# Optimization experiments

Hardware: AMD Instinct MI355X
Metric: run time of the kernel (lower is better)

Reference implementation:

```python
import jax, jax.numpy as jnp
import numpy as np

B, SQ, SK, D, H = 2, 2048, 2048, 1024, 16
DK = D // H


def setup_inputs() -> dict:
    key = jax.random.key(0)
    ks = jax.random.split(key, 9)
    query = jax.random.normal(ks[0], (B, SQ, D), dtype=jnp.float32)
    k_in = jax.random.normal(ks[1], (B, SK, D), dtype=jnp.float32)
    v_in = jax.random.normal(ks[2], (B, SK, D), dtype=jnp.float32)
    # padding mask: 1 for valid tokens, 0 for padding; lengths in [SK//2, SK]
    lengths = jax.random.randint(ks[3], (B,), SK // 2, SK + 1)
    mask = (jnp.arange(SK)[None, :] < lengths[:, None]).astype(jnp.int32)
    scale = 1.0 / np.sqrt(D)
    Wq = jax.random.normal(ks[4], (D, D), dtype=jnp.float32) * scale
    Wk = jax.random.normal(ks[5], (D, D), dtype=jnp.float32) * scale
    Wv = jax.random.normal(ks[6], (D, D), dtype=jnp.float32) * scale
    Wo = jax.random.normal(ks[7], (D, D), dtype=jnp.float32) * scale
    return {"query": query, "key": k_in, "value": v_in, "mask": mask,
            "Wq": Wq, "Wk": Wk, "Wv": Wv, "Wo": Wo}


def reference(query, key, value, mask, Wq, Wk, Wv, Wo):
    # linear projections (torch Linear: x @ W.T)
    q = (query @ Wq.T).reshape(B, SQ, H, DK).transpose(0, 2, 1, 3)  # [B,H,SQ,DK]
    k = (key @ Wk.T).reshape(B, SK, H, DK).transpose(0, 2, 1, 3)    # [B,H,SK,DK]
    v = (value @ Wv.T).reshape(B, SK, H, DK).transpose(0, 2, 1, 3)  # [B,H,SK,DK]
    scores = jnp.einsum('bhqd,bhkd->bhqk', q, k) / jnp.sqrt(jnp.float32(DK))
    # padding mask: (B, SK) -> (B, 1, 1, SK)
    scores = jnp.where(mask[:, None, None, :] == 0, -jnp.inf, scores)
    # future (causal) mask
    future = jnp.triu(jnp.ones((SQ, SK), dtype=bool), k=1)
    scores = jnp.where(future[None, None], -jnp.inf, scores)
    attn = jax.nn.softmax(scores, axis=-1)
    attn = jnp.nan_to_num(attn, nan=0.0)
    ctx = jnp.einsum('bhqk,bhkd->bhqd', attn, v)
    ctx = ctx.transpose(0, 2, 1, 3).reshape(B, SQ, D)
    return ctx @ Wo.T
```

## Files before the change

### kernel.cpp

```cpp
#include <hip/hip_runtime.h>
#include <hip/hip_bf16.h>
#include <stdint.h>

#define BB 2
#define SS 2048
#define DD 1024
#define HH 16
#define DKK 64
#define MM (BB*SS)
#define LOG2E 1.4426950408889634f
#define QSCALE (0.125f * LOG2E)

typedef __attribute__((ext_vector_type(8))) short short8;
typedef __attribute__((ext_vector_type(4))) float f32x4;

__device__ __forceinline__ short bfr(float f) {
    return (short)((__float_as_uint(f) + 0x8000u) >> 16);
}
__device__ __forceinline__ short8 cvt8(float4 a, float4 b) {
    short8 s;
    s[0] = bfr(a.x); s[1] = bfr(a.y); s[2] = bfr(a.z); s[3] = bfr(a.w);
    s[4] = bfr(b.x); s[5] = bfr(b.y); s[6] = bfr(b.z); s[7] = bfr(b.w);
    return s;
}

__device__ __forceinline__ void dma16(const void* g, void* l) {
    __builtin_amdgcn_global_load_lds(
        (const __attribute__((address_space(1))) uint32_t*)g,
        (__attribute__((address_space(3))) uint32_t*)(uintptr_t)l, 16, 0, 0);
}


__global__ __launch_bounds__(256) void cvt_all(const float* __restrict__ q,
                                               const float* __restrict__ k,
                                               const float* __restrict__ v,
                                               const float* __restrict__ wq,
                                               const float* __restrict__ wk,
                                               const float* __restrict__ wv,
                                               const float* __restrict__ wo,
                                               const int* __restrict__ mask,
                                               short* __restrict__ dst,
                                               float* __restrict__ Fb) {
    const size_t nth = (size_t)gridDim.x * blockDim.x;
    const size_t tid = (size_t)blockIdx.x * blockDim.x + threadIdx.x;
    if (tid < BB * SS) Fb[tid] = mask[tid] ? 0.f : -30000.f;
    for (size_t i8 = tid; i8 < (1u << 21); i8 += nth) {
        const size_t e = i8 * 8;
        const float* s;
        size_t rel;
        if (e < 4194304)        { s = q; rel = e; }
        else if (e < 8388608)   { s = k; rel = e - 4194304; }
        else if (e < 12582912)  { s = v; rel = e - 8388608; }
        else {
            const size_t we = e - 12582912;
            s = (we < 1048576) ? wq : (we < 2097152) ? wk : (we < 3145728) ? wv : wo;
            rel = we & 1048575;
        }
        const float4* p = (const float4*)(s + rel);
        *(short8*)(dst + e) = cvt8(p[0], p[1]);
    }
}

__global__ __launch_bounds__(256) void qkv_lds(const short* __restrict__ Abf,
                                               const short* __restrict__ Wbf,
                                               short* __restrict__ Qb,
                                               short* __restrict__ Kb,
                                               short* __restrict__ Vtb) {
    __shared__ __align__(16) short As[128 * 64];
    __shared__ __align__(16) short Ws[128 * 64];
    const int z = blockIdx.z;
    const short* A = Abf + (size_t)z * 4194304;
    const short* W = Wbf + (size_t)z * 1048576;
    const int t = threadIdx.x, wave = t >> 6, lane = t & 63;
    const int la = lane & 15, quad = lane >> 4;
    const int wm = wave & 1, wn = wave >> 1;
    const int m0 = blockIdx.x * 128, n0 = blockIdx.y * 128;

    f32x4 acc[4][4];
    #pragma unroll
    for (int i = 0; i < 4; ++i)
        #pragma unroll
        for (int j = 0; j < 4; ++j) acc[i][j] = {0.f, 0.f, 0.f, 0.f};

    for (int k0 = 0; k0 < DD; k0 += 64) {
        #pragma unroll
        for (int j = 0; j < 4; ++j) {
            const int idx = j * 256 + t;
            const int row = idx >> 3, cpos = idx & 7;
            const int gc = cpos ^ (row & 7);
            dma16(A + (size_t)(m0 + row) * DD + k0 + gc * 8, (short*)As + idx * 8);
            dma16(W + (size_t)(n0 + row) * DD + k0 + gc * 8, (short*)Ws + idx * 8);
        }
        __syncthreads();
        #pragma unroll
        for (int kh = 0; kh < 2; ++kh) {
            short8 af[4], bf[4];
            #pragma unroll
            for (int mt = 0; mt < 4; ++mt) {
                const int row = wm * 64 + mt * 16 + la;
                af[mt] = *(const short8*)&As[row * 64 + (((kh << 2) | quad) ^ (row & 7)) * 8];
            }
            #pragma unroll
            for (int nt = 0; nt < 4; ++nt) {
                const int row = wn * 64 + nt * 16 + la;
                bf[nt] = *(const short8*)&Ws[row * 64 + (((kh << 2) | quad) ^ (row & 7)) * 8];
            }
            #pragma unroll
            for (int mt = 0; mt < 4; ++mt)
                #pragma unroll
                for (int nt = 0; nt < 4; ++nt)
                    acc[mt][nt] = __builtin_amdgcn_mfma_f32_16x16x32_bf16(af[mt], bf[nt], acc[mt][nt], 0, 0, 0);
        }
        __syncthreads();
    }

    #pragma unroll
    for (int mt = 0; mt < 4; ++mt)
        #pragma unroll
        for (int nt = 0; nt < 4; ++nt)
            #pragma unroll
            for (int r = 0; r < 4; ++r) {
                const int m = m0 + wm * 64 + mt * 16 + quad * 4 + r;
                const int n = n0 + wn * 64 + nt * 16 + la;
                const int b = m >> 11, s = m & (SS - 1);
                const int h = n >> 6, dk = n & 63;
                const int bh = b * HH + h;
                const float v = acc[mt][nt][r];
                if (z == 0)      Qb[((size_t)bh * SS + s) * DKK + dk] = bfr(v * QSCALE);
                else if (z == 1) Kb[((size_t)bh * SS + s) * DKK + dk] = bfr(v);
                else             Vtb[((size_t)bh * DKK + dk) * SS + s] = bfr(v);
            }
}

__global__ __launch_bounds__(256) void attn3(const short* __restrict__ Q,
                                             const short* __restrict__ K,
                                             const short* __restrict__ Vt,
                                             const float* __restrict__ Fb,
                                             short* __restrict__ ctx) {
    const int b = blockIdx.z, h = blockIdx.y;
    const int qt = 31 - blockIdx.x;
    const int t = threadIdx.x, wave = t >> 6, lane = t & 63;
    const int la = lane & 15, quad = lane >> 4;

    __shared__ __align__(16) short Ks[64][72];
    __shared__ __align__(16) short Vs[64][72];
    __shared__ __align__(16) short Ps[64][72];

    const size_t kbase = ((size_t)(b * HH + h) * SS) * DKK;
    const size_t vbase = ((size_t)(b * HH + h) * DKK) * SS;

    const short8 aq0 = *(const short8*)(Q + kbase + (size_t)(qt * 64 + wave * 16 + la) * DKK + quad * 8);
    const short8 aq1 = *(const short8*)(Q + kbase + (size_t)(qt * 64 + wave * 16 + la) * DKK + 32 + quad * 8);

    const int srow = t >> 2, scol = (t & 3) * 16;
    short8 kr[2], vr[2];
    auto loadG = [&](int kt) {
        const short* kp = K + kbase + (size_t)(kt * 64 + srow) * DKK + scol;
        kr[0] = ((const short8*)kp)[0]; kr[1] = ((const short8*)kp)[1];
        const short* vp = Vt + vbase + (size_t)srow * SS + kt * 64 + scol;
        vr[0] = ((const short8*)vp)[0]; vr[1] = ((const short8*)vp)[1];
    };
    auto storeL = [&]() {
        *(short8*)&Ks[srow][scol]     = kr[0];
        *(short8*)&Ks[srow][scol + 8] = kr[1];
        *(short8*)&Vs[srow][scol]     = vr[0];
        *(short8*)&Vs[srow][scol + 8] = vr[1];
    };

    float rs[4] = {0.f, 0.f, 0.f, 0.f};
    f32x4 o[4];
    #pragma unroll
    for (int dc = 0; dc < 4; ++dc) o[dc] = {0.f, 0.f, 0.f, 0.f};

    loadG(0); storeL(); __syncthreads();

    for (int kt = 0; kt <= qt; ++kt) {
        if (kt < qt) loadG(kt + 1);
        const bool diag   = (kt == qt);
        const bool padded = (kt >= 16);

        f32x4 s[4];
        #pragma unroll
        for (int ct = 0; ct < 4; ++ct) {
            s[ct] = {0.f, 0.f, 0.f, 0.f};
            short8 kb0 = *(const short8*)&Ks[ct * 16 + la][quad * 8];
            short8 kb1 = *(const short8*)&Ks[ct * 16 + la][32 + quad * 8];
            s[ct] = __builtin_amdgcn_mfma_f32_16x16x32_bf16(aq0, kb0, s[ct], 0, 0, 0);
            s[ct] = __builtin_amdgcn_mfma_f32_16x16x32_bf16(aq1, kb1, s[ct], 0, 0, 0);
        }

        const int rowq = qt * 64 + wave * 16 + quad * 4;
        #pragma unroll
        for (int ct = 0; ct < 4; ++ct) {
            const int col = kt * 64 + ct * 16 + la;
            const float bias = padded ? Fb[b * SS + col] : 0.f;
            #pragma unroll
            for (int r = 0; r < 4; ++r) {
                float sv = s[ct][r] + bias;
                if (diag && col > rowq + r) sv = -30000.f;
                const float p = exp2f(sv);
                rs[r] += p;
                Ps[wave * 16 + quad * 4 + r][ct * 16 + la] = bfr(p);
            }
        }

        #pragma unroll
        for (int c2 = 0; c2 < 2; ++c2) {
            short8 pa = *(const short8*)&Ps[wave * 16 + la][c2 * 32 + quad * 8];
            #pragma unroll
            for (int dc = 0; dc < 4; ++dc) {
                short8 vb = *(const short8*)&Vs[dc * 16 + la][c2 * 32 + quad * 8];
                o[dc] = __builtin_amdgcn_mfma_f32_16x16x32_bf16(pa, vb, o[dc], 0, 0, 0);
            }
        }

        if (kt < qt) {
            __syncthreads();
            storeL();
            __syncthreads();
        }
    }

    #pragma unroll
    for (int r = 0; r < 4; ++r) {
        float v = rs[r];
        v += __shfl_xor(v, 1, 64);
        v += __shfl_xor(v, 2, 64);
        v += __shfl_xor(v, 4, 64);
        v += __shfl_xor(v, 8, 64);
        const float inv = 1.0f / v;
        const int q = qt * 64 + wave * 16 + quad * 4 + r;
        #pragma unroll
        for (int dc = 0; dc < 4; ++dc)
            ctx[((size_t)(b * SS + q) * DD) + h * DKK + dc * 16 + la] = bfr(o[dc][r] * inv);
    }
}

__global__ __launch_bounds__(256) void o_lds(const short* __restrict__ Ctx,
                                             const short* __restrict__ Wob,
                                             float* __restrict__ out) {
    __shared__ __align__(16) short As[128 * 64];
    __shared__ __align__(16) short Ws[64 * 64];
    const int t = threadIdx.x, wave = t >> 6, lane = t & 63;
    const int la = lane & 15, quad = lane >> 4;
    const int wm = wave & 1, wn = wave >> 1;
    const int m0 = blockIdx.x * 128, n0 = blockIdx.y * 64;

    f32x4 acc[4][2];
    #pragma unroll
    for (int i = 0; i < 4; ++i)
        #pragma unroll
        for (int j = 0; j < 2; ++j) acc[i][j] = {0.f, 0.f, 0.f, 0.f};

    for (int k0 = 0; k0 < DD; k0 += 64) {
        #pragma unroll
        for (int j = 0; j < 4; ++j) {
            const int idx = j * 256 + t;
            const int row = idx >> 3, cpos = idx & 7;
            const int gc = cpos ^ (row & 7);
            dma16(Ctx + (size_t)(m0 + row) * DD + k0 + gc * 8, (short*)As + idx * 8);
        }
        #pragma unroll
        for (int j = 0; j < 2; ++j) {
            const int idx = j * 256 + t;
            const int row = idx >> 3, cpos = idx & 7;
            const int gc = cpos ^ (row & 7);
            dma16(Wob + (size_t)(n0 + row) * DD + k0 + gc * 8, (short*)Ws + idx * 8);
        }
        __syncthreads();
        #pragma unroll
        for (int kh = 0; kh < 2; ++kh) {
            short8 af[4], bf[2];
            #pragma unroll
            for (int mt = 0; mt < 4; ++mt) {
                const int row = wm * 64 + mt * 16 + la;
                af[mt] = *(const short8*)&As[row * 64 + (((kh << 2) | quad) ^ (row & 7)) * 8];
            }
            #pragma unroll
            for (int nt = 0; nt < 2; ++nt) {
                const int row = wn * 32 + nt * 16 + la;
                bf[nt] = *(const short8*)&Ws[row * 64 + (((kh << 2) | quad) ^ (row & 7)) * 8];
            }
            #pragma unroll
            for (int mt = 0; mt < 4; ++mt)
                #pragma unroll
                for (int nt = 0; nt < 2; ++nt)
                    acc[mt][nt] = __builtin_amdgcn_mfma_f32_16x16x32_bf16(af[mt], bf[nt], acc[mt][nt], 0, 0, 0);
        }
        __syncthreads();
    }

    #pragma unroll
    for (int mt = 0; mt < 4; ++mt)
        #pragma unroll
        for (int nt = 0; nt < 2; ++nt)
            #pragma unroll
            for (int r = 0; r < 4; ++r) {
                const int m = m0 + wm * 64 + mt * 16 + quad * 4 + r;
                const int n = n0 + wn * 32 + nt * 16 + la;
                out[(size_t)m * DD + n] = acc[mt][nt][r];
            }
}

__global__ __launch_bounds__(256) void qkv_gemm(const float* __restrict__ Aq,
                                                const float* __restrict__ Ak,
                                                const float* __restrict__ Av,
                                                const float* __restrict__ Wq,
                                                const float* __restrict__ Wk,
                                                const float* __restrict__ Wv,
                                                short* __restrict__ Qb,
                                                short* __restrict__ Kb,
                                                short* __restrict__ Vtb) {
    __shared__ __align__(16) short As[2][128][40];
    __shared__ __align__(16) short Ws[2][128][40];
    const int z = blockIdx.z;
    const float* A = (z == 0) ? Aq : (z == 1) ? Ak : Av;
    const float* W = (z == 0) ? Wq : (z == 1) ? Wk : Wv;
    short* Y = (z == 0) ? Qb : (z == 1) ? Kb : Vtb;
    const int t = threadIdx.x, wave = t >> 6, lane = t & 63;
    const int la = lane & 15, quad = lane >> 4;
    const int wm = wave & 1, wn = wave >> 1;
    const int m0 = blockIdx.x * 128, n0 = blockIdx.y * 128;
    const int srow = t >> 1, scol = (t & 1) * 16;
    f32x4 acc[4][4];
    #pragma unroll
    for (int i = 0; i < 4; ++i)
        #pragma unroll
        for (int j = 0; j < 4; ++j) acc[i][j] = {0.f, 0.f, 0.f, 0.f};
    float4 ar[4], wr[4];
    auto loadG = [&](int i) {
        const int k0 = i * 32;
        const float4* pa = (const float4*)(A + (size_t)(m0 + srow) * DD + k0 + scol);
        ar[0] = pa[0]; ar[1] = pa[1]; ar[2] = pa[2]; ar[3] = pa[3];
        const float4* pw = (const float4*)(W + (size_t)(n0 + srow) * DD + k0 + scol);
        wr[0] = pw[0]; wr[1] = pw[1]; wr[2] = pw[2]; wr[3] = pw[3];
    };
    auto storeL = [&](int buf) {
        *(short8*)&As[buf][srow][scol]     = cvt8(ar[0], ar[1]);
        *(short8*)&As[buf][srow][scol + 8] = cvt8(ar[2], ar[3]);
        *(short8*)&Ws[buf][srow][scol]     = cvt8(wr[0], wr[1]);
        *(short8*)&Ws[buf][srow][scol + 8] = cvt8(wr[2], wr[3]);
    };
    loadG(0); storeL(0); __syncthreads();
    const int NIT = DD / 32;
    for (int i = 0; i < NIT; ++i) {
        if (i + 1 < NIT) loadG(i + 1);
        const int buf = i & 1;
        short8 af[4], bfv[4];
        #pragma unroll
        for (int mt = 0; mt < 4; ++mt)
            af[mt] = *(const short8*)&As[buf][wm * 64 + mt * 16 + la][quad * 8];
        #pragma unroll
        for (int nt = 0; nt < 4; ++nt)
            bfv[nt] = *(const short8*)&Ws[buf][wn * 64 + nt * 16 + la][quad * 8];
        #pragma unroll
        for (int mt = 0; mt < 4; ++mt)
            #pragma unroll
            for (int nt = 0; nt < 4; ++nt)
                acc[mt][nt] = __builtin_amdgcn_mfma_f32_16x16x32_bf16(af[mt], bfv[nt], acc[mt][nt], 0, 0, 0);
        if (i + 1 < NIT) { storeL((i + 1) & 1); __syncthreads(); }
    }
    #pragma unroll
    for (int mt = 0; mt < 4; ++mt)
        #pragma unroll
        for (int nt = 0; nt < 4; ++nt)
            #pragma unroll
            for (int r = 0; r < 4; ++r) {
                const int m = m0 + wm * 64 + mt * 16 + quad * 4 + r;
                const int n = n0 + wn * 64 + nt * 16 + la;
                const int b = m >> 11, s = m & (SS - 1);
                const int h = n >> 6, dk = n & 63;
                float v = acc[mt][nt][r];
                if (z == 0)      Y[(((size_t)(b * HH + h) * SS + s) * DKK) + dk] = bfr(v * QSCALE);
                else if (z == 1) Y[(((size_t)(b * HH + h) * SS + s) * DKK) + dk] = bfr(v);
                else             Y[(((size_t)(b * HH + h) * DKK + dk) * SS) + s] = bfr(v);
            }
}

__global__ __launch_bounds__(256) void attn_fused(const short* __restrict__ Q,
                                                  const short* __restrict__ K,
                                                  const short* __restrict__ Vt,
                                                  const int* __restrict__ mask,
                                                  short* __restrict__ ctx) {
    const int b = blockIdx.z, h = blockIdx.y, x = blockIdx.x;
    const int t = threadIdx.x, wave = t >> 6, lane = t & 63;
    const int la = lane & 15, quad = lane >> 4;
    __shared__ __align__(16) short Ks[2][64][72];
    __shared__ __align__(16) short Vs[2][64][72];
    __shared__ __align__(16) short Ps[64][72];
    const size_t kbase = ((size_t)(b * HH + h) * SS) * DKK;
    const size_t vbase = ((size_t)(b * HH + h) * DKK) * SS;
    const int srow = t >> 2, scol = (t & 3) * 16;
    short8 kr[2], vr[2];
    auto loadG = [&](int kt) {
        const short* kp = K + kbase + (size_t)(kt * 64 + srow) * DKK + scol;
        kr[0] = ((const short8*)kp)[0]; kr[1] = ((const short8*)kp)[1];
        const short* vp = Vt + vbase + (size_t)srow * SS + kt * 64 + scol;
        vr[0] = ((const short8*)vp)[0]; vr[1] = ((const short8*)vp)[1];
    };
    auto storeL = [&](int buf) {
        *(short8*)&Ks[buf][srow][scol]     = kr[0];
        *(short8*)&Ks[buf][srow][scol + 8] = kr[1];
        *(short8*)&Vs[buf][srow][scol]     = vr[0];
        *(short8*)&Vs[buf][srow][scol + 8] = vr[1];
    };
    #pragma unroll 1
    for (int phase = 0; phase < 2; ++phase) {
        const int qt = phase ? x : (31 - x);
        const size_t qbase = kbase + (size_t)(qt * 64) * DKK;
        const short8 aq0 = *(const short8*)(Q + qbase + (size_t)(wave * 16 + la) * DKK + quad * 8);
        const short8 aq1 = *(const short8*)(Q + qbase + (size_t)(wave * 16 + la) * DKK + 32 + quad * 8);
        float rs[4] = {0.f, 0.f, 0.f, 0.f};
        f32x4 o[4];
        #pragma unroll
        for (int dc = 0; dc < 4; ++dc) o[dc] = {0.f, 0.f, 0.f, 0.f};
        const int nkt = qt + 1;
        loadG(0); storeL(0); __syncthreads();
        for (int kt = 0; kt < nkt; ++kt) {
            if (kt + 1 < nkt) loadG(kt + 1);
            const int buf = kt & 1;
            const bool diag = (kt == qt);
            const bool padded = (kt >= 16);
            f32x4 s[4];
            #pragma unroll
            for (int ct = 0; ct < 4; ++ct) {
                s[ct] = {0.f, 0.f, 0.f, 0.f};
                short8 kb0 = *(const short8*)&Ks[buf][ct * 16 + la][quad * 8];
                short8 kb1 = *(const short8*)&Ks[buf][ct * 16 + la][32 + quad * 8];
                s[ct] = __builtin_amdgcn_mfma_f32_16x16x32_bf16(aq0, kb0, s[ct], 0, 0, 0);
                s[ct] = __builtin_amdgcn_mfma_f32_16x16x32_bf16(aq1, kb1, s[ct], 0, 0, 0);
            }
            const int rowq = qt * 64 + wave * 16 + quad * 4;
            #pragma unroll
            for (int ct = 0; ct < 4; ++ct) {
                const int col = kt * 64 + ct * 16 + la;
                const int mv = padded ? mask[b * SS + col] : 1;
                #pragma unroll
                for (int r = 0; r < 4; ++r) {
                    const bool dead = (diag && col > rowq + r) || (padded && mv == 0);
                    const float p = dead ? 0.f : exp2f(s[ct][r]);
                    rs[r] += p;
                    Ps[wave * 16 + quad * 4 + r][ct * 16 + la] = bfr(p);
                }
            }
            #pragma unroll
            for (int c2 = 0; c2 < 2; ++c2) {
                short8 pa = *(const short8*)&Ps[wave * 16 + la][c2 * 32 + quad * 8];
                #pragma unroll
                for (int dc = 0; dc < 4; ++dc) {
                    short8 vb = *(const short8*)&Vs[buf][dc * 16 + la][c2 * 32 + quad * 8];
                    o[dc] = __builtin_amdgcn_mfma_f32_16x16x32_bf16(pa, vb, o[dc], 0, 0, 0);
                }
            }
            if (kt + 1 < nkt) { storeL((kt + 1) & 1); __syncthreads(); }
        }
        #pragma unroll
        for (int r = 0; r < 4; ++r) {
            float v = rs[r];
            v += __shfl_xor(v, 1, 64);
            v += __shfl_xor(v, 2, 64);
            v += __shfl_xor(v, 4, 64);
            v += __shfl_xor(v, 8, 64);
            const float inv = 1.0f / v;
            const int q = qt * 64 + wave * 16 + quad * 4 + r;
            #pragma unroll
            for (int dc = 0; dc < 4; ++dc)
                ctx[((size_t)(b * SS + q) * DD) + h * DKK + dc * 16 + la] = bfr(o[dc][r] * inv);
        }
        __syncthreads();
    }
}

__global__ __launch_bounds__(256) void o_gemm(const short* __restrict__ Ctx,
                                              const float* __restrict__ Wo,
                                              float* __restrict__ out) {
    __shared__ __align__(16) short As[2][128][40];
    __shared__ __align__(16) short Ws[2][64][40];
    const int t = threadIdx.x, wave = t >> 6, lane = t & 63;
    const int la = lane & 15, quad = lane >> 4;
    const int wm = wave & 1, wn = wave >> 1;
    const int m0 = blockIdx.x * 128, n0 = blockIdx.y * 64;
    const int srowA = t >> 1, scolA = (t & 1) * 16;
    const int srowW = t >> 2, scolW = (t & 3) * 8;
    f32x4 acc[4][2];
    #pragma unroll
    for (int i = 0; i < 4; ++i)
        #pragma unroll
        for (int j = 0; j < 2; ++j) acc[i][j] = {0.f, 0.f, 0.f, 0.f};
    short8 ab[2];
    float4 wr[2];
    auto loadG = [&](int i) {
        const int k0 = i * 32;
        const short8* pa = (const short8*)(Ctx + (size_t)(m0 + srowA) * DD + k0 + scolA);
        ab[0] = pa[0]; ab[1] = pa[1];
        const float4* pw = (const float4*)(Wo + (size_t)(n0 + srowW) * DD + k0 + scolW);
        wr[0] = pw[0]; wr[1] = pw[1];
    };
    auto storeL = [&](int buf) {
        *(short8*)&As[buf][srowA][scolA]     = ab[0];
        *(short8*)&As[buf][srowA][scolA + 8] = ab[1];
        *(short8*)&Ws[buf][srowW][scolW]     = cvt8(wr[0], wr[1]);
    };
    loadG(0); storeL(0); __syncthreads();
    const int NIT = DD / 32;
    for (int i = 0; i < NIT; ++i) {
        if (i + 1 < NIT) loadG(i + 1);
        const int buf = i & 1;
        short8 af[4], bfv[2];
        #pragma unroll
        for (int mt = 0; mt < 4; ++mt)
            af[mt] = *(const short8*)&As[buf][wm * 64 + mt * 16 + la][quad * 8];
        #pragma unroll
        for (int nt = 0; nt < 2; ++nt)
            bfv[nt] = *(const short8*)&Ws[buf][wn * 32 + nt * 16 + la][quad * 8];
        #pragma unroll
        for (int mt = 0; mt < 4; ++mt)
            #pragma unroll
            for (int nt = 0; nt < 2; ++nt)
                acc[mt][nt] = __builtin_amdgcn_mfma_f32_16x16x32_bf16(af[mt], bfv[nt], acc[mt][nt], 0, 0, 0);
        if (i + 1 < NIT) { storeL((i + 1) & 1); __syncthreads(); }
    }
    #pragma unroll
    for (int mt = 0; mt < 4; ++mt)
        #pragma unroll
        for (int nt = 0; nt < 2; ++nt)
            #pragma unroll
            for (int r = 0; r < 4; ++r) {
                const int m = m0 + wm * 64 + mt * 16 + quad * 4 + r;
                const int n = n0 + wn * 32 + nt * 16 + la;
                out[(size_t)m * DD + n] = acc[mt][nt][r];
            }
}

extern "C" void kernel_launch(void* const* d_in, const int* in_sizes, int n_in,
                              void* d_out, int out_size, void* d_ws, size_t ws_size,
                              hipStream_t stream) {
    (void)in_sizes; (void)n_in; (void)out_size;
    const float* query = (const float*)d_in[0];
    const float* key   = (const float*)d_in[1];
    const float* value = (const float*)d_in[2];
    const int*   mask  = (const int*)  d_in[3];
    const float* Wq    = (const float*)d_in[4];
    const float* Wk    = (const float*)d_in[5];
    const float* Wv    = (const float*)d_in[6];
    const float* Wo    = (const float*)d_in[7];
    dim3 tb(256);

    if (ws_size >= (size_t)61000000) {
        short* Abf = (short*)d_ws;
        short* Wbf = Abf + 12582912;
        short* Qb  = Abf + 16777216;
        short* Kb  = Abf + 20971520;
        short* Vtb = Abf + 25165824;
        float* Fb  = (float*)(Abf + 29360128);
        short* Ctx = Abf;

        hipLaunchKernelGGL(cvt_all, dim3(1024), tb, 0, stream,
                           query, key, value, Wq, Wk, Wv, Wo, mask, Abf, Fb);
        hipLaunchKernelGGL(qkv_lds, dim3(32, 8, 3), tb, 0, stream, Abf, Wbf, Qb, Kb, Vtb);
        hipLaunchKernelGGL(attn3, dim3(32, 16, 2), tb, 0, stream,
                           (const short*)Qb, (const short*)Kb, (const short*)Vtb, Fb, Ctx);
        hipLaunchKernelGGL(o_lds, dim3(32, 16), tb, 0, stream,
                           (const short*)Ctx, (const short*)(Wbf + 3145728), (float*)d_out);
    } else {
        short* Qb  = (short*)d_ws;
        short* Kb  = Qb + (size_t)BB * HH * SS * DKK;
        short* Vtb = Kb + (size_t)BB * HH * SS * DKK;
        short* Ctx = Vtb + (size_t)BB * HH * SS * DKK;
        hipLaunchKernelGGL(qkv_gemm, dim3(MM / 128, DD / 128, 3), tb, 0, stream,
                           query, key, value, Wq, Wk, Wv, Qb, Kb, Vtb);
        hipLaunchKernelGGL(attn_fused, dim3(SS / 128, HH, BB), tb, 0, stream,
                           (const short*)Qb, (const short*)Kb, (const short*)Vtb, mask, Ctx);
        hipLaunchKernelGGL(o_gemm, dim3(MM / 128, DD / 64), tb, 0, stream,
                           (const short*)Ctx, Wo, (float*)d_out);
    }
}
```

Measured before the change: 264.8 us.

## Stage QKV epilogue through LDS and double attention query tile to 128

The QKV GEMM epilogue now writes its accumulators into shared memory and then issues coalesced 16-byte global stores, transposing V in LDS instead of scattering scalar stores. The attention kernel processes 128 query rows per block (two 16-row tiles per wave), so each K/V tile loaded into LDS is reused twice as much and the block count is halved. P and V are switched to fp16 with f16 MFMA for the PV product, which gives more mantissa than bf16. Risks include fewer blocks and worse load balance under the causal mask, higher register pressure, and V held in fp16 could overflow for large values.

```diff
diff --git a/kernel.cpp b/kernel.cpp
--- a/kernel.cpp
+++ b/kernel.cpp
@@ -12,10 +12,15 @@
 #define QSCALE (0.125f * LOG2E)
 
 typedef __attribute__((ext_vector_type(8))) short short8;
+typedef __attribute__((ext_vector_type(8))) _Float16 half8;
 typedef __attribute__((ext_vector_type(4))) float f32x4;
 
 __device__ __forceinline__ short bfr(float f) {
     return (short)((__float_as_uint(f) + 0x8000u) >> 16);
+}
+__device__ __forceinline__ short f2h(float f) {
+    _Float16 h = (_Float16)f;
+    return __builtin_bit_cast(short, h);
 }
 __device__ __forceinline__ short8 cvt8(float4 a, float4 b) {
     short8 s;
@@ -66,8 +71,9 @@
                                                short* __restrict__ Qb,
                                                short* __restrict__ Kb,
                                                short* __restrict__ Vtb) {
-    __shared__ __align__(16) short As[128 * 64];
-    __shared__ __align__(16) short Ws[128 * 64];
+    __shared__ __align__(16) short SH[128 * 132];
+    short* As = SH;
+    short* Ws = SH + 8192;
     const int z = blockIdx.z;
     const short* A = Abf + (size_t)z * 4194304;
     const short* W = Wbf + (size_t)z * 1048576;
@@ -88,8 +94,8 @@
             const int idx = j * 256 + t;
             const int row = idx >> 3, cpos = idx & 7;
             const int gc = cpos ^ (row & 7);
-            dma16(A + (size_t)(m0 + row) * DD + k0 + gc * 8, (short*)As + idx * 8);
-            dma16(W + (size_t)(n0 + row) * DD + k0 + gc * 8, (short*)Ws + idx * 8);
+            dma16(A + (size_t)(m0 + row) * DD + k0 + gc * 8, As + idx * 8);
+            dma16(W + (size_t)(n0 + row) * DD + k0 + gc * 8, Ws + idx * 8);
         }
         __syncthreads();
         #pragma unroll
@@ -120,37 +126,57 @@
         for (int nt = 0; nt < 4; ++nt)
             #pragma unroll
             for (int r = 0; r < 4; ++r) {
-                const int m = m0 + wm * 64 + mt * 16 + quad * 4 + r;
-                const int n = n0 + wn * 64 + nt * 16 + la;
-                const int b = m >> 11, s = m & (SS - 1);
-                const int h = n >> 6, dk = n & 63;
-                const int bh = b * HH + h;
                 const float v = acc[mt][nt][r];
-                if (z == 0)      Qb[((size_t)bh * SS + s) * DKK + dk] = bfr(v * QSCALE);
-                else if (z == 1) Kb[((size_t)bh * SS + s) * DKK + dk] = bfr(v);
-                else             Vtb[((size_t)bh * DKK + dk) * SS + s] = bfr(v);
-            }
-}
-
-__global__ __launch_bounds__(256) void attn3(const short* __restrict__ Q,
-                                             const short* __restrict__ K,
-                                             const short* __restrict__ Vt,
-                                             const float* __restrict__ Fb,
-                                             short* __restrict__ ctx) {
+                const int mr = wm * 64 + mt * 16 + quad * 4 + r;
+                const int nc = wn * 64 + nt * 16 + la;
+                if (z == 2) SH[nc * 132 + mr] = f2h(v);
+                else        SH[mr * 132 + nc] = bfr(z == 0 ? v * QSCALE : v);
+            }
+    __syncthreads();
+
+    const int b = m0 >> 11;
+    #pragma unroll
+    for (int p = 0; p < 8; ++p) {
+        const int idx = p * 256 + t;
+        const int rr = idx >> 4, c8 = (idx & 15) * 8;
+        short8 val = *(const short8*)&SH[rr * 132 + c8];
+        if (z == 2) {
+            const int n = n0 + rr, h2 = n >> 6, dk = n & 63;
+            const int s = (m0 & 2047) + c8;
+            *(short8*)(Vtb + ((size_t)(b * HH + h2) * DKK + dk) * SS + s) = val;
+        } else {
+            const int s = (m0 + rr) & 2047;
+            const int n = n0 + c8, h2 = n >> 6, dk = n & 63;
+            short* Y = (z == 0) ? Qb : Kb;
+            *(short8*)(Y + ((size_t)(b * HH + h2) * SS + s) * DKK + dk) = val;
+        }
+    }
+}
+
+__global__ __launch_bounds__(256, 4) void attn4(const short* __restrict__ Q,
+                                                const short* __restrict__ K,
+                                                const short* __restrict__ Vt,
+                                                const float* __restrict__ Fb,
+                                                short* __restrict__ ctx) {
     const int b = blockIdx.z, h = blockIdx.y;
-    const int qt = 31 - blockIdx.x;
+    const int qt = 15 - blockIdx.x;
     const int t = threadIdx.x, wave = t >> 6, lane = t & 63;
     const int la = lane & 15, quad = lane >> 4;
 
-    __shared__ __align__(16) short Ks[64][72];
-    __shared__ __align__(16) short Vs[64][72];
-    __shared__ __align__(16) short Ps[64][72];
+    __shared__ __align__(16) short Ks[64 * 72];
+    __shared__ __align__(16) short Vs[64 * 72];
+    __shared__ __align__(16) short Ps[128 * 76];
 
     const size_t kbase = ((size_t)(b * HH + h) * SS) * DKK;
     const size_t vbase = ((size_t)(b * HH + h) * DKK) * SS;
 
-    const short8 aq0 = *(const short8*)(Q + kbase + (size_t)(qt * 64 + wave * 16 + la) * DKK + quad * 8);
-    const short8 aq1 = *(const short8*)(Q + kbase + (size_t)(qt * 64 + wave * 16 + la) * DKK + 32 + quad * 8);
+    short8 aq[2][2];
+    #pragma unroll
+    for (int mt = 0; mt < 2; ++mt)
+        #pragma unroll
+        for (int hf = 0; hf < 2; ++hf)
+            aq[mt][hf] = *(const short8*)(Q + kbase
+                + (size_t)(qt * 128 + wave * 32 + mt * 16 + la) * DKK + hf * 32 + quad * 8);
 
     const int srow = t >> 2, scol = (t & 3) * 16;
     short8 kr[2], vr[2];
@@ -161,60 +187,67 @@
         vr[0] = ((const short8*)vp)[0]; vr[1] = ((const short8*)vp)[1];
     };
     auto storeL = [&]() {
-        *(short8*)&Ks[srow][scol]     = kr[0];
-        *(short8*)&Ks[srow][scol + 8] = kr[1];
-        *(short8*)&Vs[srow][scol]     = vr[0];
-        *(short8*)&Vs[srow][scol + 8] = vr[1];
-    };
-
-    float rs[4] = {0.f, 0.f, 0.f, 0.f};
-    f32x4 o[4];
-    #pragma unroll
-    for (int dc = 0; dc < 4; ++dc) o[dc] = {0.f, 0.f, 0.f, 0.f};
-
+        *(short8*)&Ks[srow * 72 + scol]     = kr[0];
+        *(short8*)&Ks[srow * 72 + scol + 8] = kr[1];
+        *(short8*)&Vs[srow * 72 + scol]     = vr[0];
+        *(short8*)&Vs[srow * 72 + scol + 8] = vr[1];
+    };
+
+    float rs[2][4] = {};
+    f32x4 o[2][4];
+    #pragma unroll
+    for (int mt = 0; mt < 2; ++mt)
+        #pragma unroll
+        for (int dc = 0; dc < 4; ++dc) o[mt][dc] = {0.f, 0.f, 0.f, 0.f};
+
+    const int lastkt = 2 * qt + 1;
     loadG(0); storeL(); __syncthreads();
 
-    for (int kt = 0; kt <= qt; ++kt) {
-        if (kt < qt) loadG(kt + 1);
-        const bool diag   = (kt == qt);
+    for (int kt = 0; kt <= lastkt; ++kt) {
+        if (kt < lastkt) loadG(kt + 1);
+        const bool diag   = (kt >= 2 * qt);
         const bool padded = (kt >= 16);
 
-        f32x4 s[4];
         #pragma unroll
         for (int ct = 0; ct < 4; ++ct) {
-            s[ct] = {0.f, 0.f, 0.f, 0.f};
-            short8 kb0 = *(const short8*)&Ks[ct * 16 + la][quad * 8];
-            short8 kb1 = *(const short8*)&Ks[ct * 16 + la][32 + quad * 8];
-            s[ct] = __builtin_amdgcn_mfma_f32_16x16x32_bf16(aq0, kb0, s[ct], 0, 0, 0);
-            s[ct] = __builtin_amdgcn_mfma_f32_16x16x32_bf16(aq1, kb1, s[ct], 0, 0, 0);
-        }
-
-        const int rowq = qt * 64 + wave * 16 + quad * 4;
-        #pragma unroll
-        for (int ct = 0; ct < 4; ++ct) {
+            short8 kb0 = *(const short8*)&Ks[(ct * 16 + la) * 72 + quad * 8];
+            short8 kb1 = *(const short8*)&Ks[(ct * 16 + la) * 72 + 32 + quad * 8];
+            f32x4 s[2];
+            #pragma unroll
+            for (int mt = 0; mt < 2; ++mt) {
+                s[mt] = {0.f, 0.f, 0.f, 0.f};
+                s[mt] = __builtin_amdgcn_mfma_f32_16x16x32_bf16(aq[mt][0], kb0, s[mt], 0, 0, 0);
+                s[mt] = __builtin_amdgcn_mfma_f32_16x16x32_bf16(aq[mt][1], kb1, s[mt], 0, 0, 0);
+            }
             const int col = kt * 64 + ct * 16 + la;
             const float bias = padded ? Fb[b * SS + col] : 0.f;
             #pragma unroll
-            for (int r = 0; r < 4; ++r) {
-                float sv = s[ct][r] + bias;
-                if (diag && col > rowq + r) sv = -30000.f;
-                const float p = exp2f(sv);
-                rs[r] += p;
-                Ps[wave * 16 + quad * 4 + r][ct * 16 + la] = bfr(p);
+            for (int mt = 0; mt < 2; ++mt) {
+                const int row0 = qt * 128 + wave * 32 + mt * 16 + quad * 4;
+                #pragma unroll
+                for (int r = 0; r < 4; ++r) {
+                    float x = s[mt][r] + bias;
+                    if (diag && col > row0 + r) x = -30000.f;
+                    const float p = exp2f(x);
+                    rs[mt][r] += p;
+                    Ps[(wave * 32 + mt * 16 + quad * 4 + r) * 76 + ct * 16 + la] = f2h(p);
+                }
             }
         }
 
         #pragma unroll
         for (int c2 = 0; c2 < 2; ++c2) {
-            short8 pa = *(const short8*)&Ps[wave * 16 + la][c2 * 32 + quad * 8];
+            half8 pa0 = *(const half8*)&Ps[(wave * 32 + la) * 76 + c2 * 32 + quad * 8];
+            half8 pa1 = *(const half8*)&Ps[(wave * 32 + 16 + la) * 76 + c2 * 32 + quad * 8];
             #pragma unroll
             for (int dc = 0; dc < 4; ++dc) {
-                short8 vb = *(const short8*)&Vs[dc * 16 + la][c2 * 32 + quad * 8];
-                o[dc] = __builtin_amdgcn_mfma_f32_16x16x32_bf16(pa, vb, o[dc], 0, 0, 0);
-            }
-        }
-
-        if (kt < qt) {
+                half8 vb = *(const half8*)&Vs[(dc * 16 + la) * 72 + c2 * 32 + quad * 8];
+                o[0][dc] = __builtin_amdgcn_mfma_f32_16x16x32_f16(pa0, vb, o[0][dc], 0, 0, 0);
+                o[1][dc] = __builtin_amdgcn_mfma_f32_16x16x32_f16(pa1, vb, o[1][dc], 0, 0, 0);
+            }
+        }
+
+        if (kt < lastkt) {
             __syncthreads();
             storeL();
             __syncthreads();
@@ -222,17 +255,20 @@
     }
 
     #pragma unroll
-    for (int r = 0; r < 4; ++r) {
-        float v = rs[r];
-        v += __shfl_xor(v, 1, 64);
-        v += __shfl_xor(v, 2, 64);
-        v += __shfl_xor(v, 4, 64);
-        v += __shfl_xor(v, 8, 64);
-        const float inv = 1.0f / v;
-        const int q = qt * 64 + wave * 16 + quad * 4 + r;
-        #pragma unroll
-        for (int dc = 0; dc < 4; ++dc)
-            ctx[((size_t)(b * SS + q) * DD) + h * DKK + dc * 16 + la] = bfr(o[dc][r] * inv);
+    for (int mt = 0; mt < 2; ++mt) {
+        #pragma unroll
+        for (int r = 0; r < 4; ++r) {
+            float v = rs[mt][r];
+            v += __shfl_xor(v, 1, 64);
+            v += __shfl_xor(v, 2, 64);
+            v += __shfl_xor(v, 4, 64);
+            v += __shfl_xor(v, 8, 64);
+            const float inv = 1.0f / v;
+            const int q = qt * 128 + wave * 32 + mt * 16 + quad * 4 + r;
+            #pragma unroll
+            for (int dc = 0; dc < 4; ++dc)
+                ctx[((size_t)(b * SS + q) * DD) + h * DKK + dc * 16 + la] = bfr(o[mt][dc][r] * inv);
+        }
     }
 }
 
@@ -558,7 +594,7 @@
         hipLaunchKernelGGL(cvt_all, dim3(1024), tb, 0, stream,
                            query, key, value, Wq, Wk, Wv, Wo, mask, Abf, Fb);
         hipLaunchKernelGGL(qkv_lds, dim3(32, 8, 3), tb, 0, stream, Abf, Wbf, Qb, Kb, Vtb);
-        hipLaunchKernelGGL(attn3, dim3(32, 16, 2), tb, 0, stream,
+        hipLaunchKernelGGL(attn4, dim3(16, 16, 2), tb, 0, stream,
                            (const short*)Qb, (const short*)Kb, (const short*)Vtb, Fb, Ctx);
         hipLaunchKernelGGL(o_lds, dim3(32, 16), tb, 0, stream,
                            (const short*)Ctx, (const short*)(Wbf + 3145728), (float*)d_out);
```

Result: slower. 286.2 us (+8.1%).
